# Kernel tuning notes

Hardware: AMD Instinct MI355X
Metric: run time of the kernel (lower is better)

Reference implementation:

```python
import jax, jax.numpy as jnp
import numpy as np

N_NODES = 100000
N_EDGES = 3200000
C = 256
NEG_SLOPE = 0.2


def setup_inputs() -> dict:
    key = jax.random.key(0)
    k1, k2, k3, k4 = jax.random.split(key, 4)
    x = jax.random.normal(k1, (N_NODES, C), dtype=jnp.float32)
    # xavier_uniform on (2C, 1): bound = sqrt(6/(2C+1))
    bound = float(np.sqrt(6.0 / (2 * C + 1)))
    att = jax.random.uniform(k2, (2 * C, 1), dtype=jnp.float32, minval=-bound, maxval=bound)
    row = jax.random.randint(k3, (N_EDGES,), 0, N_NODES, dtype=jnp.int64)
    col = jax.random.randint(k4, (N_EDGES,), 0, N_NODES, dtype=jnp.int64)
    edge_index = jnp.stack([row, col], axis=0)
    return {"x": x, "att": att, "edge_index": edge_index}


def reference(x, att, edge_index):
    # Original: alpha = leaky_relu(cat([x[row], x[col]], -1) @ att)
    # Equivalent split form avoids materializing the [E, 2C] concat:
    # alpha_e = (x @ att[:C])[row] + (x @ att[C:])[col]
    row, col = edge_index[0], edge_index[1]
    n = x.shape[0]
    c = x.shape[1]
    s_src = (x @ att[:c]).squeeze(-1)  # (N,)
    s_dst = (x @ att[c:]).squeeze(-1)  # (N,)
    alpha = jax.nn.leaky_relu(s_src[row] + s_dst[col], negative_slope=NEG_SLOPE)  # (E,)
    # scatter_softmax over edges grouped by destination row id
    m = jax.ops.segment_max(alpha, row, num_segments=n)          # (N,)
    e = jnp.exp(alpha - m[row])                                   # (E,)
    denom = jax.ops.segment_sum(e, row, num_segments=n)          # (N,)
    out = e / denom[row]                                          # (E,)
    # torch code transposes [E,1] -> [1,E] before scatter_softmax; squeeze(-1) is a no-op
    return out[None, :]
```

## Files before the change

### kernel.cpp

```cpp
#include <hip/hip_runtime.h>

#define NN 100000
#define NE 3200000
#define CC 256
#define NEG_SLOPE 0.2f

#define SEG_S 32
#define SEG_P 8
#define PART_SZ 12500
#define SEG_BLOCK 1024
#define ESLICE (NE / SEG_S)

typedef __attribute__((ext_vector_type(8))) _Float16 half8;

__global__ __launch_bounds__(256) void node_scores_kernel(
    const float* __restrict__ x,
    const float* __restrict__ att,
    float* __restrict__ s_src,
    float* __restrict__ s_dst) {
  int gid  = blockIdx.x * blockDim.x + threadIdx.x;
  int node = gid >> 6;
  int lane = threadIdx.x & 63;
  if (node >= NN) return;
  const float4* xr = (const float4*)(x + (size_t)node * CC);
  const float4* a0 = (const float4*)att;
  const float4* a1 = (const float4*)(att + CC);
  float4 xv = xr[lane];
  float4 av = a0[lane];
  float4 bv = a1[lane];
  float s0 = xv.x * av.x + xv.y * av.y + xv.z * av.z + xv.w * av.w;
  float s1 = xv.x * bv.x + xv.y * bv.y + xv.z * bv.z + xv.w * bv.w;
#pragma unroll
  for (int off = 32; off > 0; off >>= 1) {
    s0 += __shfl_down(s0, off, 64);
    s1 += __shfl_down(s1, off, 64);
  }
  if (lane == 0) {
    s_src[node] = s0;
    s_dst[node] = s1;
  }
}

__global__ __launch_bounds__(256) void edge_exp_kernel(
    const int4* __restrict__ row4,
    const int4* __restrict__ col4,
    const float* __restrict__ s_src,
    const float* __restrict__ s_dst,
    half8* __restrict__ e_out) {
  int i = blockIdx.x * blockDim.x + threadIdx.x;
  if (i >= NE / 8) return;
  int4 ra = row4[2 * i], rb = row4[2 * i + 1];
  int4 ca = col4[2 * i], cb = col4[2 * i + 1];
  float a0 = s_src[ra.x] + s_dst[ca.x];
  float a1 = s_src[ra.y] + s_dst[ca.y];
  float a2 = s_src[ra.z] + s_dst[ca.z];
  float a3 = s_src[ra.w] + s_dst[ca.w];
  float a4 = s_src[rb.x] + s_dst[cb.x];
  float a5 = s_src[rb.y] + s_dst[cb.y];
  float a6 = s_src[rb.z] + s_dst[cb.z];
  float a7 = s_src[rb.w] + s_dst[cb.w];
  a0 = (a0 > 0.0f) ? a0 : NEG_SLOPE * a0;
  a1 = (a1 > 0.0f) ? a1 : NEG_SLOPE * a1;
  a2 = (a2 > 0.0f) ? a2 : NEG_SLOPE * a2;
  a3 = (a3 > 0.0f) ? a3 : NEG_SLOPE * a3;
  a4 = (a4 > 0.0f) ? a4 : NEG_SLOPE * a4;
  a5 = (a5 > 0.0f) ? a5 : NEG_SLOPE * a5;
  a6 = (a6 > 0.0f) ? a6 : NEG_SLOPE * a6;
  a7 = (a7 > 0.0f) ? a7 : NEG_SLOPE * a7;
  half8 h;
  h[0] = (_Float16)__expf(a0);
  h[1] = (_Float16)__expf(a1);
  h[2] = (_Float16)__expf(a2);
  h[3] = (_Float16)__expf(a3);
  h[4] = (_Float16)__expf(a4);
  h[5] = (_Float16)__expf(a5);
  h[6] = (_Float16)__expf(a6);
  h[7] = (_Float16)__expf(a7);
  e_out[i] = h;
}

__global__ __launch_bounds__(SEG_BLOCK) void segsum_kernel(
    const int* __restrict__ row,
    const _Float16* __restrict__ e,
    float* __restrict__ partial ) {
  __shared__ float lds[PART_SZ];
  int s = blockIdx.x;
  int p = blockIdx.y;
  for (int i = threadIdx.x; i < PART_SZ; i += SEG_BLOCK) lds[i] = 0.0f;
  __syncthreads();
  int lo = p * PART_SZ;
  const int4*  row4 = (const int4*)(row + s * ESLICE);
  const half8* e8   = (const half8*)(e + (size_t)s * ESLICE);
  const int n8 = ESLICE / 8;
  for (int i = threadIdx.x; i < n8; i += SEG_BLOCK) {
    int4 ra = row4[2 * i], rb = row4[2 * i + 1];
    half8 ev = e8[i];
    int r0 = ra.x - lo; if ((unsigned)r0 < PART_SZ) atomicAdd(&lds[r0], (float)ev[0]);
    int r1 = ra.y - lo; if ((unsigned)r1 < PART_SZ) atomicAdd(&lds[r1], (float)ev[1]);
    int r2 = ra.z - lo; if ((unsigned)r2 < PART_SZ) atomicAdd(&lds[r2], (float)ev[2]);
    int r3 = ra.w - lo; if ((unsigned)r3 < PART_SZ) atomicAdd(&lds[r3], (float)ev[3]);
    int r4 = rb.x - lo; if ((unsigned)r4 < PART_SZ) atomicAdd(&lds[r4], (float)ev[4]);
    int r5 = rb.y - lo; if ((unsigned)r5 < PART_SZ) atomicAdd(&lds[r5], (float)ev[5]);
    int r6 = rb.z - lo; if ((unsigned)r6 < PART_SZ) atomicAdd(&lds[r6], (float)ev[6]);
    int r7 = rb.w - lo; if ((unsigned)r7 < PART_SZ) atomicAdd(&lds[r7], (float)ev[7]);
  }
  __syncthreads();
  float* outp = partial + (size_t)s * NN + lo;
  for (int i = threadIdx.x; i < PART_SZ; i += SEG_BLOCK) outp[i] = lds[i];
}

__global__ __launch_bounds__(256) void reduce_kernel(
    const float* __restrict__ partial,
    float* __restrict__ denom) {
  int n4 = blockIdx.x * blockDim.x + threadIdx.x;
  if (n4 >= NN / 4) return;
  float4 sum = make_float4(0.f, 0.f, 0.f, 0.f);
#pragma unroll
  for (int s = 0; s < SEG_S; ++s) {
    float4 v = ((const float4*)(partial + (size_t)s * NN))[n4];
    sum.x += v.x; sum.y += v.y; sum.z += v.z; sum.w += v.w;
  }
  ((float4*)denom)[n4] = make_float4(1.f / sum.x, 1.f / sum.y, 1.f / sum.z, 1.f / sum.w);
}

__global__ __launch_bounds__(256) void edge_div_kernel(
    const int4* __restrict__ row4,
    const half8* __restrict__ e,
    const float* __restrict__ denom,
    float4* __restrict__ out4) {
  int i = blockIdx.x * blockDim.x + threadIdx.x;
  if (i >= NE / 8) return;
  int4 ra = row4[2 * i], rb = row4[2 * i + 1];
  half8 ev = e[i];
  float4 oa, ob;
  oa.x = (float)ev[0] * denom[ra.x];
  oa.y = (float)ev[1] * denom[ra.y];
  oa.z = (float)ev[2] * denom[ra.z];
  oa.w = (float)ev[3] * denom[ra.w];
  ob.x = (float)ev[4] * denom[rb.x];
  ob.y = (float)ev[5] * denom[rb.y];
  ob.z = (float)ev[6] * denom[rb.z];
  ob.w = (float)ev[7] * denom[rb.w];
  out4[2 * i]     = oa;
  out4[2 * i + 1] = ob;
}

extern "C" void kernel_launch(void* const* d_in, const int* in_sizes, int n_in,
                              void* d_out, int out_size, void* d_ws, size_t ws_size,
                              hipStream_t stream) {
  const float* x   = (const float*)d_in[0];
  const float* att = (const float*)d_in[1];
  const int* ei    = (const int*)d_in[2];
  const int* row   = ei;
  const int4* row4 = (const int4*)ei;
  const int4* col4 = (const int4*)(ei + NE);
  float4* out4     = (float4*)d_out;

  float* s_src      = (float*)d_ws;
  float* s_dst      = s_src + NN;
  float* denom      = s_dst + NN;
  _Float16* e_buf   = (_Float16*)(denom + NN);
  float* partial    = (float*)(e_buf + NE);

  node_scores_kernel<<<(NN * 64 + 255) / 256, 256, 0, stream>>>(x, att, s_src, s_dst);
  edge_exp_kernel<<<(NE / 8 + 255) / 256, 256, 0, stream>>>(
      row4, col4, s_src, s_dst, (half8*)e_buf);
  dim3 seg_grid(SEG_S, SEG_P);
  segsum_kernel<<<seg_grid, SEG_BLOCK, 0, stream>>>(row, e_buf, partial);
  reduce_kernel<<<(NN / 4 + 255) / 256, 256, 0, stream>>>(partial, denom);
  edge_div_kernel<<<(NE / 8 + 255) / 256, 256, 0, stream>>>(
      row4, (const half8*)e_buf, denom, out4);
}
```

Before: 235.4 us.

## Store segment partials in fp16, grid-stride node scores, nontemporal edge loads/stores

Several unrelated changes. Node scores now use a fixed grid of waves that stride over nodes and load att once per wave. The per-slice segment-sum partials are stored as fp16 rather than fp32, halving partial write and read traffic, and the reduction reads them eight at a time with nontemporal loads. The final edge kernel uses nontemporal loads and stores for the streaming row, exp and output arrays. The fp16 partials lose precision on the denominator sums and could overflow when a row's partial sum is large.

```diff
diff --git a/kernel.cpp b/kernel.cpp
--- a/kernel.cpp
+++ b/kernel.cpp
@@ -12,32 +12,29 @@
 #define ESLICE (NE / SEG_S)
 
 typedef __attribute__((ext_vector_type(8))) _Float16 half8;
+typedef __attribute__((ext_vector_type(4))) float f32x4;
+typedef __attribute__((ext_vector_type(4))) int i32x4;
 
 __global__ __launch_bounds__(256) void node_scores_kernel(
     const float* __restrict__ x,
     const float* __restrict__ att,
     float* __restrict__ s_src,
     float* __restrict__ s_dst) {
-  int gid  = blockIdx.x * blockDim.x + threadIdx.x;
-  int node = gid >> 6;
+  int wave = (blockIdx.x * blockDim.x + threadIdx.x) >> 6;
   int lane = threadIdx.x & 63;
-  if (node >= NN) return;
-  const float4* xr = (const float4*)(x + (size_t)node * CC);
-  const float4* a0 = (const float4*)att;
-  const float4* a1 = (const float4*)(att + CC);
-  float4 xv = xr[lane];
-  float4 av = a0[lane];
-  float4 bv = a1[lane];
-  float s0 = xv.x * av.x + xv.y * av.y + xv.z * av.z + xv.w * av.w;
-  float s1 = xv.x * bv.x + xv.y * bv.y + xv.z * bv.z + xv.w * bv.w;
+  const int nwaves = (gridDim.x * blockDim.x) >> 6;
+  float4 av = ((const float4*)att)[lane];
+  float4 bv = ((const float4*)(att + CC))[lane];
+  for (int node = wave; node < NN; node += nwaves) {
+    float4 xv = ((const float4*)(x + (size_t)node * CC))[lane];
+    float s0 = xv.x * av.x + xv.y * av.y + xv.z * av.z + xv.w * av.w;
+    float s1 = xv.x * bv.x + xv.y * bv.y + xv.z * bv.z + xv.w * bv.w;
 #pragma unroll
-  for (int off = 32; off > 0; off >>= 1) {
-    s0 += __shfl_down(s0, off, 64);
-    s1 += __shfl_down(s1, off, 64);
-  }
-  if (lane == 0) {
-    s_src[node] = s0;
-    s_dst[node] = s1;
+    for (int off = 32; off > 0; off >>= 1) {
+      s0 += __shfl_down(s0, off, 64);
+      s1 += __shfl_down(s1, off, 64);
+    }
+    if (lane == 0) { s_src[node] = s0; s_dst[node] = s1; }
   }
 }
 
@@ -82,67 +79,72 @@
 __global__ __launch_bounds__(SEG_BLOCK) void segsum_kernel(
     const int* __restrict__ row,
     const _Float16* __restrict__ e,
-    float* __restrict__ partial ) {
-  __shared__ float lds[PART_SZ];
-  int s = blockIdx.x;
-  int p = blockIdx.y;
-  for (int i = threadIdx.x; i < PART_SZ; i += SEG_BLOCK) lds[i] = 0.0f;
+    _Float16* __restrict__ partial ) {
+  __shared__ float tile[PART_SZ];
+  const int s = blockIdx.x;
+  const int p = blockIdx.y;
+  for (int i = threadIdx.x; i < PART_SZ; i += SEG_BLOCK) tile[i] = 0.0f;
   __syncthreads();
-  int lo = p * PART_SZ;
-  const int4*  row4 = (const int4*)(row + s * ESLICE);
-  const half8* e8   = (const half8*)(e + (size_t)s * ESLICE);
-  const int n8 = ESLICE / 8;
-  for (int i = threadIdx.x; i < n8; i += SEG_BLOCK) {
-    int4 ra = row4[2 * i], rb = row4[2 * i + 1];
+  const int lo = p * PART_SZ;
+  const int4*  row4s = (const int4*)(row + s * ESLICE);
+  const half8* e8    = (const half8*)(e + (size_t)s * ESLICE);
+  for (int i = threadIdx.x; i < ESLICE / 8; i += SEG_BLOCK) {
+    int4 ra = row4s[2 * i], rb = row4s[2 * i + 1];
     half8 ev = e8[i];
-    int r0 = ra.x - lo; if ((unsigned)r0 < PART_SZ) atomicAdd(&lds[r0], (float)ev[0]);
-    int r1 = ra.y - lo; if ((unsigned)r1 < PART_SZ) atomicAdd(&lds[r1], (float)ev[1]);
-    int r2 = ra.z - lo; if ((unsigned)r2 < PART_SZ) atomicAdd(&lds[r2], (float)ev[2]);
-    int r3 = ra.w - lo; if ((unsigned)r3 < PART_SZ) atomicAdd(&lds[r3], (float)ev[3]);
-    int r4 = rb.x - lo; if ((unsigned)r4 < PART_SZ) atomicAdd(&lds[r4], (float)ev[4]);
-    int r5 = rb.y - lo; if ((unsigned)r5 < PART_SZ) atomicAdd(&lds[r5], (float)ev[5]);
-    int r6 = rb.z - lo; if ((unsigned)r6 < PART_SZ) atomicAdd(&lds[r6], (float)ev[6]);
-    int r7 = rb.w - lo; if ((unsigned)r7 < PART_SZ) atomicAdd(&lds[r7], (float)ev[7]);
+    int r0 = ra.x - lo; if ((unsigned)r0 < PART_SZ) atomicAdd(&tile[r0], (float)ev[0]);
+    int r1 = ra.y - lo; if ((unsigned)r1 < PART_SZ) atomicAdd(&tile[r1], (float)ev[1]);
+    int r2 = ra.z - lo; if ((unsigned)r2 < PART_SZ) atomicAdd(&tile[r2], (float)ev[2]);
+    int r3 = ra.w - lo; if ((unsigned)r3 < PART_SZ) atomicAdd(&tile[r3], (float)ev[3]);
+    int r4 = rb.x - lo; if ((unsigned)r4 < PART_SZ) atomicAdd(&tile[r4], (float)ev[4]);
+    int r5 = rb.y - lo; if ((unsigned)r5 < PART_SZ) atomicAdd(&tile[r5], (float)ev[5]);
+    int r6 = rb.z - lo; if ((unsigned)r6 < PART_SZ) atomicAdd(&tile[r6], (float)ev[6]);
+    int r7 = rb.w - lo; if ((unsigned)r7 < PART_SZ) atomicAdd(&tile[r7], (float)ev[7]);
   }
   __syncthreads();
-  float* outp = partial + (size_t)s * NN + lo;
-  for (int i = threadIdx.x; i < PART_SZ; i += SEG_BLOCK) outp[i] = lds[i];
+  _Float16* outp = partial + (size_t)s * NN + lo;
+  for (int i = threadIdx.x; i < PART_SZ; i += SEG_BLOCK)
+    outp[i] = (_Float16)tile[i];
 }
 
 __global__ __launch_bounds__(256) void reduce_kernel(
-    const float* __restrict__ partial,
-    float* __restrict__ denom) {
-  int n4 = blockIdx.x * blockDim.x + threadIdx.x;
-  if (n4 >= NN / 4) return;
-  float4 sum = make_float4(0.f, 0.f, 0.f, 0.f);
+    const _Float16* __restrict__ partial,
+    float* __restrict__ rdenom) {
+  int n8 = blockIdx.x * blockDim.x + threadIdx.x;
+  if (n8 >= NN / 8) return;
+  float sum[8] = {0, 0, 0, 0, 0, 0, 0, 0};
 #pragma unroll
   for (int s = 0; s < SEG_S; ++s) {
-    float4 v = ((const float4*)(partial + (size_t)s * NN))[n4];
-    sum.x += v.x; sum.y += v.y; sum.z += v.z; sum.w += v.w;
+    half8 v = __builtin_nontemporal_load(
+        &((const half8*)(partial + (size_t)s * NN))[n8]);
+#pragma unroll
+    for (int k = 0; k < 8; ++k) sum[k] += (float)v[k];
   }
-  ((float4*)denom)[n4] = make_float4(1.f / sum.x, 1.f / sum.y, 1.f / sum.z, 1.f / sum.w);
+  int n = 8 * n8;
+#pragma unroll
+  for (int k = 0; k < 8; ++k) rdenom[n + k] = 1.0f / sum[k];
 }
 
 __global__ __launch_bounds__(256) void edge_div_kernel(
-    const int4* __restrict__ row4,
+    const i32x4* __restrict__ row4,
     const half8* __restrict__ e,
-    const float* __restrict__ denom,
-    float4* __restrict__ out4) {
+    const float* __restrict__ rdenom,
+    f32x4* __restrict__ out4) {
   int i = blockIdx.x * blockDim.x + threadIdx.x;
   if (i >= NE / 8) return;
-  int4 ra = row4[2 * i], rb = row4[2 * i + 1];
-  half8 ev = e[i];
-  float4 oa, ob;
-  oa.x = (float)ev[0] * denom[ra.x];
-  oa.y = (float)ev[1] * denom[ra.y];
-  oa.z = (float)ev[2] * denom[ra.z];
-  oa.w = (float)ev[3] * denom[ra.w];
-  ob.x = (float)ev[4] * denom[rb.x];
-  ob.y = (float)ev[5] * denom[rb.y];
-  ob.z = (float)ev[6] * denom[rb.z];
-  ob.w = (float)ev[7] * denom[rb.w];
-  out4[2 * i]     = oa;
-  out4[2 * i + 1] = ob;
+  i32x4 ra = __builtin_nontemporal_load(&row4[2 * i]);
+  i32x4 rb = __builtin_nontemporal_load(&row4[2 * i + 1]);
+  half8 ev = __builtin_nontemporal_load(&e[i]);
+  f32x4 oa, ob;
+  oa.x = (float)ev[0] * rdenom[ra.x];
+  oa.y = (float)ev[1] * rdenom[ra.y];
+  oa.z = (float)ev[2] * rdenom[ra.z];
+  oa.w = (float)ev[3] * rdenom[ra.w];
+  ob.x = (float)ev[4] * rdenom[rb.x];
+  ob.y = (float)ev[5] * rdenom[rb.y];
+  ob.z = (float)ev[6] * rdenom[rb.z];
+  ob.w = (float)ev[7] * rdenom[rb.w];
+  __builtin_nontemporal_store(oa, &out4[2 * i]);
+  __builtin_nontemporal_store(ob, &out4[2 * i + 1]);
 }
 
 extern "C" void kernel_launch(void* const* d_in, const int* in_sizes, int n_in,
@@ -152,22 +154,22 @@
   const float* att = (const float*)d_in[1];
   const int* ei    = (const int*)d_in[2];
   const int* row   = ei;
-  const int4* row4 = (const int4*)ei;
+  const int4* row4 = (const int4*)row;
   const int4* col4 = (const int4*)(ei + NE);
-  float4* out4     = (float4*)d_out;
+  f32x4* out4      = (f32x4*)d_out;
 
-  float* s_src      = (float*)d_ws;
-  float* s_dst      = s_src + NN;
-  float* denom      = s_dst + NN;
-  _Float16* e_buf   = (_Float16*)(denom + NN);
-  float* partial    = (float*)(e_buf + NE);
+  float* s_src     = (float*)d_ws;
+  float* s_dst     = s_src + NN;
+  float* rdenom    = s_dst + NN;
+  _Float16* e_buf  = (_Float16*)(rdenom + NN);
+  _Float16* partial = e_buf + NE;
 
-  node_scores_kernel<<<(NN * 64 + 255) / 256, 256, 0, stream>>>(x, att, s_src, s_dst);
+  node_scores_kernel<<<1600, 256, 0, stream>>>(x, att, s_src, s_dst);
   edge_exp_kernel<<<(NE / 8 + 255) / 256, 256, 0, stream>>>(
       row4, col4, s_src, s_dst, (half8*)e_buf);
   dim3 seg_grid(SEG_S, SEG_P);
   segsum_kernel<<<seg_grid, SEG_BLOCK, 0, stream>>>(row, e_buf, partial);
-  reduce_kernel<<<(NN / 4 + 255) / 256, 256, 0, stream>>>(partial, denom);
+  reduce_kernel<<<(NN / 8 + 255) / 256, 256, 0, stream>>>(partial, rdenom);
   edge_div_kernel<<<(NE / 8 + 255) / 256, 256, 0, stream>>>(
-      row4, (const half8*)e_buf, denom, out4);
+      (const i32x4*)row4, (const half8*)e_buf, rdenom, out4);
 }
```

Result: slower. 240.8 us (+2.3%).
